# Kernel tuning notes

Hardware: AMD Instinct MI355X
Metric: run time of the kernel (lower is better)

## Reference

```python
import jax, jax.numpy as jnp
import numpy as np

HIDDEN = 1024
HEADS = 16
HEAD = HIDDEN // HEADS
B, S = 2, 2048


def setup_inputs() -> dict:
    key = jax.random.key(0)
    ks = jax.random.split(key, 8)
    query = jax.random.normal(ks[0], (B, S, HIDDEN), dtype=jnp.float32)
    key_t = jax.random.normal(ks[1], (B, S, HIDDEN), dtype=jnp.float32)
    value = jax.random.normal(ks[2], (B, S, HIDDEN), dtype=jnp.float32)
    # causal mask, broadcastable over batch and heads; 0 -> masked (-inf)
    mask = jnp.tril(jnp.ones((S, S), dtype=jnp.int32))[None, None, :, :]
    # torch Linear weights are [out_features, in_features]
    scale = 0.02
    Wq = jax.random.normal(ks[3], (HIDDEN, HIDDEN), dtype=jnp.float32) * scale
    Wk = jax.random.normal(ks[4], (HIDDEN, HIDDEN), dtype=jnp.float32) * scale
    Wv = jax.random.normal(ks[5], (HIDDEN, HIDDEN), dtype=jnp.float32) * scale
    Wo = jax.random.normal(ks[6], (HIDDEN, HIDDEN), dtype=jnp.float32) * scale
    bo = jax.random.normal(ks[7], (HIDDEN,), dtype=jnp.float32) * scale
    return {"query": query, "key": key_t, "value": value, "mask": mask,
            "Wq": Wq, "Wk": Wk, "Wv": Wv, "Wo": Wo, "bo": bo}


def reference(query, key, value, mask, Wq, Wk, Wv, Wo, bo):
    b = query.shape[0]
    # Linear (no bias): x @ W^T, then split into heads -> [b, h, s, d]
    def heads(x, W):
        y = jnp.einsum('bse,oe->bso', x, W)
        return y.reshape(b, -1, HEADS, HEAD).transpose(0, 2, 1, 3)
    Q = heads(query, Wq)
    K = heads(key, Wk)
    V = heads(value, Wv)
    inv_scale = 1.0 / jnp.sqrt(jnp.float32(HEAD))
    scores = jnp.einsum('bhqd,bhkd->bhqk', Q, K) * inv_scale  # [b,h,s,s]
    scores = jnp.where(mask == 0, -jnp.inf, scores)
    attn = jax.nn.softmax(scores, axis=-1)
    x = jnp.einsum('bhqk,bhkd->bhqd', attn, V)
    x = x.transpose(0, 2, 1, 3).reshape(b, -1, HIDDEN)
    return jnp.einsum('bse,oe->bso', x, Wo) + bo
```

## Files before the change

### kernel.cpp

```cpp
#include <hip/hip_runtime.h>


typedef __attribute__((ext_vector_type(8))) short short8;
typedef __attribute__((ext_vector_type(4))) short short4_;
typedef __attribute__((ext_vector_type(4))) float f32x4;
typedef unsigned int u32;
typedef unsigned short u16;

__device__ inline f32x4 mfma16(short8 a, short8 b, f32x4 c) {
    return __builtin_amdgcn_mfma_f32_16x16x32_bf16(a, b, c, 0, 0, 0);
}
__device__ inline u16 f2bf(float f) {
    union { float f; u32 u; } v; v.f = f;
    u32 r = v.u + 0x7fff + ((v.u >> 16) & 1);
    return (u16)(r >> 16);
}
__device__ inline void gll16(void* lds, const void* g) {
    __builtin_amdgcn_global_load_lds((const __attribute__((address_space(1))) u32*)g,
                                     (__attribute__((address_space(3))) u32*)lds,
                                     16, 0, 0);
}

__global__ __launch_bounds__(256)
void cvt_all(const float* __restrict__ q, const float* __restrict__ k,
             const float* __restrict__ v, const float* __restrict__ wq,
             const float* __restrict__ wk, const float* __restrict__ wv,
             const float* __restrict__ wo,
             u16* __restrict__ q16, u16* __restrict__ k16,
             u16* __restrict__ v16, u16* __restrict__ w16) {
    const size_t QKV = 1u << 22;
    const size_t WSZ = 1u << 20;
    size_t base = ((size_t)blockIdx.x * 256 + threadIdx.x) * 8;
    const float* src; u16* dst; size_t off; float scale = 1.0f;
    if (base < QKV)            { src = q; dst = q16; off = base;           scale = 0.125f; }
    else if (base < 2 * QKV)   { src = k; dst = k16; off = base - QKV;     }
    else if (base < 3 * QKV)   { src = v; dst = v16; off = base - 2 * QKV; }
    else {
        size_t wb = base - 3 * QKV;
        int wi = (int)(wb >> 20); off = wb & (WSZ - 1);
        src = wi == 0 ? wq : wi == 1 ? wk : wi == 2 ? wv : wo;
        dst = w16 + (size_t)wi * WSZ;
    }
    float4 f0 = *(const float4*)(src + off);
    float4 f1 = *(const float4*)(src + off + 4);
    short8 s = { (short)f2bf(f0.x * scale), (short)f2bf(f0.y * scale),
                 (short)f2bf(f0.z * scale), (short)f2bf(f0.w * scale),
                 (short)f2bf(f1.x * scale), (short)f2bf(f1.y * scale),
                 (short)f2bf(f1.z * scale), (short)f2bf(f1.w * scale) };
    *(short8*)(dst + off) = s;
}

__global__ __launch_bounds__(256)
void gemm_qkv(const u16* __restrict__ q16, const u16* __restrict__ k16,
              const u16* __restrict__ v16, const u16* __restrict__ w16,
              u16* __restrict__ Qg, u16* __restrict__ Kg, u16* __restrict__ Vt) {
    const int K = 1024;
    __shared__ u16 As[2][128 * 64];
    __shared__ u16 Bs[2][128 * 64];
    const int z = blockIdx.z;
    const u16* A = z == 0 ? q16 : z == 1 ? k16 : v16;
    const u16* W = w16 + (size_t)z * (1u << 20);

    const int tid = threadIdx.x, lane = tid & 63, w = tid >> 6;
    const int ln15 = lane & 15, quad = lane >> 4, s7 = ln15 & 7;
    const int lr = lane >> 3;
    const int lcs = (((lane & 7) ^ lr) << 3);
    const int m0 = blockIdx.y * 128, n0 = blockIdx.x * 128;
    const int wm = (w >> 1) * 64, wn = (w & 1) * 64;

    f32x4 acc[4][4] = {};

    #pragma unroll
    for (int c = 0; c < 4; ++c) {
        gll16(&As[0][(w * 32 + c * 8) * 64],
              &A[(size_t)(m0 + w * 32 + c * 8 + lr) * K + lcs]);
        gll16(&Bs[0][(w * 32 + c * 8) * 64],
              &W[(size_t)(n0 + w * 32 + c * 8 + lr) * K + lcs]);
    }

    for (int i = 0; i < 16; ++i) {
        const int cur = i & 1;
        if (i < 15) {
            const int nb = cur ^ 1, k0 = (i + 1) * 64;
            #pragma unroll
            for (int c = 0; c < 4; ++c) {
                gll16(&As[nb][(w * 32 + c * 8) * 64],
                      &A[(size_t)(m0 + w * 32 + c * 8 + lr) * K + k0 + lcs]);
                gll16(&Bs[nb][(w * 32 + c * 8) * 64],
                      &W[(size_t)(n0 + w * 32 + c * 8 + lr) * K + k0 + lcs]);
            }
            __asm__ volatile("s_waitcnt vmcnt(8)" ::: "memory");
        } else {
            __asm__ volatile("s_waitcnt vmcnt(0)" ::: "memory");
        }
        __builtin_amdgcn_s_barrier();

        #pragma unroll
        for (int kh = 0; kh < 2; ++kh) {
            short8 a[4], b[4];
            #pragma unroll
            for (int mt = 0; mt < 4; ++mt)
                a[mt] = *(const short8*)&As[cur][(wm + mt * 16 + ln15) * 64 +
                                                (((kh * 4 + quad) ^ s7) << 3)];
            #pragma unroll
            for (int nt = 0; nt < 4; ++nt)
                b[nt] = *(const short8*)&Bs[cur][(wn + nt * 16 + ln15) * 64 +
                                                (((kh * 4 + quad) ^ s7) << 3)];
            #pragma unroll
            for (int mt = 0; mt < 4; ++mt)
                #pragma unroll
                for (int nt = 0; nt < 4; ++nt)
                    acc[mt][nt] = mfma16(a[mt], b[nt], acc[mt][nt]);
        }
        __builtin_amdgcn_s_barrier();
    }

    #pragma unroll
    for (int mt = 0; mt < 4; ++mt)
        #pragma unroll
        for (int nt = 0; nt < 4; ++nt)
            #pragma unroll
            for (int r = 0; r < 4; ++r) {
                int m = m0 + wm + mt * 16 + quad * 4 + r;
                int n = n0 + wn + nt * 16 + ln15;
                u16 hv = f2bf(acc[mt][nt][r]);
                if (z == 2) {
                    int b_ = m >> 11, s_ = m & 2047, h_ = n >> 6, d_ = n & 63;
                    int kl = s_ & 63;
                    int sp = (s_ & ~63) + (kl & 15) * 4 + (kl >> 4);
                    Vt[((size_t)(b_ * 16 + h_) * 64 + d_) * 2048 + sp] = hv;
                } else {
                    u16* dst = z ? Kg : Qg;
                    dst[(size_t)m * 1024 + n] = hv;
                }
            }
}

__global__ __launch_bounds__(256)
void gemm_out(const u16* __restrict__ A, const u16* __restrict__ W,
              const float* __restrict__ bias, float* __restrict__ out) {
    const int K = 1024;
    __shared__ u16 As[2][64 * 64];
    __shared__ u16 Bs[2][128 * 64];
    const int id = blockIdx.x;
    const int by = id >> 3, bx = id & 7;

    const int tid = threadIdx.x, lane = tid & 63, w = tid >> 6;
    const int ln15 = lane & 15, quad = lane >> 4, s7 = ln15 & 7;
    const int lr = lane >> 3;
    const int lcs = (((lane & 7) ^ lr) << 3);
    const int m0 = by * 64, n0 = bx * 128;
    const int wm = (w & 1) * 32, wn = (w >> 1) * 64;

    f32x4 acc[2][4] = {};

    #pragma unroll
    for (int c = 0; c < 2; ++c)
        gll16(&As[0][(w * 16 + c * 8) * 64],
              &A[(size_t)(m0 + w * 16 + c * 8 + lr) * K + lcs]);
    #pragma unroll
    for (int c = 0; c < 4; ++c)
        gll16(&Bs[0][(w * 32 + c * 8) * 64],
              &W[(size_t)(n0 + w * 32 + c * 8 + lr) * K + lcs]);

    for (int i = 0; i < 16; ++i) {
        const int cur = i & 1;
        if (i < 15) {
            const int nb = cur ^ 1, k0 = (i + 1) * 64;
            #pragma unroll
            for (int c = 0; c < 2; ++c)
                gll16(&As[nb][(w * 16 + c * 8) * 64],
                      &A[(size_t)(m0 + w * 16 + c * 8 + lr) * K + k0 + lcs]);
            #pragma unroll
            for (int c = 0; c < 4; ++c)
                gll16(&Bs[nb][(w * 32 + c * 8) * 64],
                      &W[(size_t)(n0 + w * 32 + c * 8 + lr) * K + k0 + lcs]);
            __asm__ volatile("s_waitcnt vmcnt(6)" ::: "memory");
        } else {
            __asm__ volatile("s_waitcnt vmcnt(0)" ::: "memory");
        }
        __builtin_amdgcn_s_barrier();

        #pragma unroll
        for (int kh = 0; kh < 2; ++kh) {
            short8 a[2], b[4];
            #pragma unroll
            for (int mt = 0; mt < 2; ++mt)
                a[mt] = *(const short8*)&As[cur][(wm + mt * 16 + ln15) * 64 +
                                                (((kh * 4 + quad) ^ s7) << 3)];
            #pragma unroll
            for (int nt = 0; nt < 4; ++nt)
                b[nt] = *(const short8*)&Bs[cur][(wn + nt * 16 + ln15) * 64 +
                                                (((kh * 4 + quad) ^ s7) << 3)];
            #pragma unroll
            for (int mt = 0; mt < 2; ++mt)
                #pragma unroll
                for (int nt = 0; nt < 4; ++nt)
                    acc[mt][nt] = mfma16(a[mt], b[nt], acc[mt][nt]);
        }
        __builtin_amdgcn_s_barrier();
    }

    #pragma unroll
    for (int mt = 0; mt < 2; ++mt)
        #pragma unroll
        for (int nt = 0; nt < 4; ++nt)
            #pragma unroll
            for (int r = 0; r < 4; ++r) {
                int m = m0 + wm + mt * 16 + quad * 4 + r;
                int n = n0 + wn + nt * 16 + ln15;
                out[(size_t)m * 1024 + n] = acc[mt][nt][r] + bias[n];
            }
}

__global__ __launch_bounds__(256)
void attn3(const u16* __restrict__ Qg, const u16* __restrict__ Kg,
           const u16* __restrict__ Vt, u16* __restrict__ Xb) {
    __shared__ u16 Kl[2][64 * 64];
    __shared__ u16 Vl[2][64 * 64];
    __shared__ u16 Pl[4][16 * 72];

    const int id = blockIdx.x;
    const int bh = id & 31, qt = 31 - (id >> 5);
    const int b = bh >> 4, h = bh & 15;
    const int tid = threadIdx.x, lane = tid & 63, w = tid >> 6;
    const int ln15 = lane & 15, quad = lane >> 4, s7 = ln15 & 7;
    const int lr = lane >> 3;
    const int lcs = (((lane & 7) ^ lr) << 3);
    const u16* Kbase = Kg + (size_t)b * 2048 * 1024 + h * 64;
    const u16* Vbase = Vt + (size_t)bh * 64 * 2048;
    const float M0 = 6.0f;
    const int q0 = qt * 64;

    const u16* qrow = Qg + (size_t)(b * 2048 + q0 + w * 16 + ln15) * 1024 + h * 64;
    short8 aq0 = *(const short8*)(qrow + quad * 8);
    short8 aq1 = *(const short8*)(qrow + 32 + quad * 8);
    __asm__ volatile("s_waitcnt vmcnt(0)" ::: "memory");

    f32x4 o[4] = {};
    float lsum[4] = {0.f, 0.f, 0.f, 0.f};

    #pragma unroll
    for (int c = 0; c < 2; ++c) {
        const int r0 = w * 16 + c * 8;
        gll16(&Kl[0][r0 * 64], Kbase + (size_t)(r0 + lr) * 1024 + lcs);
        gll16(&Vl[0][r0 * 64], Vbase + (size_t)(r0 + lr) * 2048 + lcs);
    }

    for (int kt = 0; kt <= qt; ++kt) {
        const int cur = kt & 1;
        if (kt < qt) {
            const int nb = cur ^ 1, nk = (kt + 1) * 64;
            #pragma unroll
            for (int c = 0; c < 2; ++c) {
                const int r0 = w * 16 + c * 8;
                gll16(&Kl[nb][r0 * 64], Kbase + (size_t)(nk + r0 + lr) * 1024 + lcs);
                gll16(&Vl[nb][r0 * 64], Vbase + (size_t)(r0 + lr) * 2048 + nk + lcs);
            }
            __asm__ volatile("s_waitcnt vmcnt(4)" ::: "memory");
        } else {
            __asm__ volatile("s_waitcnt vmcnt(0)" ::: "memory");
        }
        __builtin_amdgcn_s_barrier();

        f32x4 sc[4];
        #pragma unroll
        for (int ct = 0; ct < 4; ++ct) {
            short8 b0 = *(const short8*)&Kl[cur][(ct * 16 + ln15) * 64 +
                                                ((quad ^ s7) << 3)];
            short8 b1 = *(const short8*)&Kl[cur][(ct * 16 + ln15) * 64 +
                                                (((4 + quad) ^ s7) << 3)];
            f32x4 c = {};
            c = mfma16(aq0, b0, c);
            c = mfma16(aq1, b1, c);
            sc[ct] = c;
        }

        const bool diag = (kt == qt);
        #pragma unroll
        for (int r = 0; r < 4; ++r) {
            float s0 = sc[0][r], s1 = sc[1][r], s2 = sc[2][r], s3 = sc[3][r];
            if (diag) {
                const int qq = w * 16 + quad * 4 + r;
                s0 = (ln15      <= qq) ? s0 : -1e30f;
                s1 = (16 + ln15 <= qq) ? s1 : -1e30f;
                s2 = (32 + ln15 <= qq) ? s2 : -1e30f;
                s3 = (48 + ln15 <= qq) ? s3 : -1e30f;
            }
            float p0 = __expf(s0 - M0), p1 = __expf(s1 - M0);
            float p2 = __expf(s2 - M0), p3 = __expf(s3 - M0);
            short4_ pw = { (short)f2bf(p0), (short)f2bf(p1),
                           (short)f2bf(p2), (short)f2bf(p3) };
            *(short4_*)&Pl[w][(quad * 4 + r) * 72 + ln15 * 4] = pw;
            lsum[r] += (p0 + p1) + (p2 + p3);
        }

        __asm__ volatile("s_waitcnt lgkmcnt(0)" ::: "memory");
        short8 ap0 = *(const short8*)&Pl[w][ln15 * 72 + quad * 8];
        short8 ap1 = *(const short8*)&Pl[w][ln15 * 72 + 32 + quad * 8];

        #pragma unroll
        for (int dt = 0; dt < 4; ++dt) {
            short8 bv0 = *(const short8*)&Vl[cur][(dt * 16 + ln15) * 64 +
                                                 ((quad ^ s7) << 3)];
            short8 bv1 = *(const short8*)&Vl[cur][(dt * 16 + ln15) * 64 +
                                                 (((4 + quad) ^ s7) << 3)];
            o[dt] = mfma16(ap0, bv0, o[dt]);
            o[dt] = mfma16(ap1, bv1, o[dt]);
        }
        __builtin_amdgcn_s_barrier();
    }

    #pragma unroll
    for (int r = 0; r < 4; ++r) {
        float l = lsum[r];
        #pragma unroll
        for (int off = 1; off < 16; off <<= 1)
            l += __shfl_xor(l, off);
        lsum[r] = l;
    }
    #pragma unroll
    for (int dt = 0; dt < 4; ++dt)
        #pragma unroll
        for (int r = 0; r < 4; ++r) {
            int q = q0 + w * 16 + quad * 4 + r;
            Xb[(size_t)(b * 2048 + q) * 1024 + h * 64 + dt * 16 + ln15] =
                f2bf(o[dt][r] / lsum[r]);
        }
}

extern "C" void kernel_launch(void* const* d_in, const int* in_sizes, int n_in,
                              void* d_out, int out_size, void* d_ws, size_t ws_size,
                              hipStream_t stream) {
    const float* query = (const float*)d_in[0];
    const float* key   = (const float*)d_in[1];
    const float* value = (const float*)d_in[2];
    const float* Wq = (const float*)d_in[4];
    const float* Wk = (const float*)d_in[5];
    const float* Wv = (const float*)d_in[6];
    const float* Wo = (const float*)d_in[7];
    const float* bo = (const float*)d_in[8];
    float* out = (float*)d_out;

    u16* ws  = (u16*)d_ws;
    const size_t T = 1ull << 22;
    u16* q16 = ws;
    u16* k16 = ws + T;
    u16* v16 = ws + 2 * T;
    u16* w16 = ws + 3 * T;
    u16* Qg  = ws + 4 * T;
    u16* Kg  = ws + 5 * T;
    u16* Vt  = (u16*)d_out;
    u16* Xb  = q16;
    const size_t WSZ = 1ull << 20;

    cvt_all<<<8192, 256, 0, stream>>>(query, key, value, Wq, Wk, Wv, Wo,
                                      q16, k16, v16, w16);

    gemm_qkv<<<dim3(8, 32, 3), 256, 0, stream>>>(q16, k16, v16, w16, Qg, Kg, Vt);

    attn3<<<1024, 256, 0, stream>>>(Qg, Kg, Vt, Xb);

    gemm_out<<<512, 256, 0, stream>>>(Xb, w16 + 3 * WSZ, bo, out);
}
```

Baseline: 230.9 us.

## Process two query tiles per attention block to reuse K/V tiles

Each attention workgroup now handles 128 query rows (two 64-row subtiles) instead of 64, so every K/V tile loaded into LDS is used by both subtiles. This halves the grid to 512 blocks and roughly halves global K/V traffic and load/barrier overhead per query row. The trade-off is fewer blocks for load balancing on a causal workload, more registers for the doubled accumulators, and serialized subtile work within each tile iteration.

```diff
diff --git a/kernel.cpp b/kernel.cpp
--- a/kernel.cpp
+++ b/kernel.cpp
@@ -214,14 +214,14 @@
 }
 
 __global__ __launch_bounds__(256)
-void attn3(const u16* __restrict__ Qg, const u16* __restrict__ Kg,
+void attn5(const u16* __restrict__ Qg, const u16* __restrict__ Kg,
            const u16* __restrict__ Vt, u16* __restrict__ Xb) {
     __shared__ u16 Kl[2][64 * 64];
     __shared__ u16 Vl[2][64 * 64];
     __shared__ u16 Pl[4][16 * 72];
 
     const int id = blockIdx.x;
-    const int bh = id & 31, qt = 31 - (id >> 5);
+    const int bh = id & 31, qt = 15 - (id >> 5);
     const int b = bh >> 4, h = bh & 15;
     const int tid = threadIdx.x, lane = tid & 63, w = tid >> 6;
     const int ln15 = lane & 15, quad = lane >> 4, s7 = ln15 & 7;
@@ -230,15 +230,20 @@
     const u16* Kbase = Kg + (size_t)b * 2048 * 1024 + h * 64;
     const u16* Vbase = Vt + (size_t)bh * 64 * 2048;
     const float M0 = 6.0f;
-    const int q0 = qt * 64;
-
-    const u16* qrow = Qg + (size_t)(b * 2048 + q0 + w * 16 + ln15) * 1024 + h * 64;
-    short8 aq0 = *(const short8*)(qrow + quad * 8);
-    short8 aq1 = *(const short8*)(qrow + 32 + quad * 8);
+    const int q0 = qt * 128;
+    const int lastkt = 2 * qt + 1;
+
+    short8 aq[2][2];
+    #pragma unroll
+    for (int s = 0; s < 2; ++s) {
+        const u16* qrow = Qg + (size_t)(b * 2048 + q0 + s * 64 + w * 16 + ln15) * 1024 + h * 64;
+        aq[s][0] = *(const short8*)(qrow + quad * 8);
+        aq[s][1] = *(const short8*)(qrow + 32 + quad * 8);
+    }
     __asm__ volatile("s_waitcnt vmcnt(0)" ::: "memory");
 
-    f32x4 o[4] = {};
-    float lsum[4] = {0.f, 0.f, 0.f, 0.f};
+    f32x4 o[2][4] = {};
+    float lsum[2][4] = {};
 
     #pragma unroll
     for (int c = 0; c < 2; ++c) {
@@ -247,9 +252,9 @@
         gll16(&Vl[0][r0 * 64], Vbase + (size_t)(r0 + lr) * 2048 + lcs);
     }
 
-    for (int kt = 0; kt <= qt; ++kt) {
+    for (int kt = 0; kt <= lastkt; ++kt) {
         const int cur = kt & 1;
-        if (kt < qt) {
+        if (kt < lastkt) {
             const int nb = cur ^ 1, nk = (kt + 1) * 64;
             #pragma unroll
             for (int c = 0; c < 2; ++c) {
@@ -263,70 +268,78 @@
         }
         __builtin_amdgcn_s_barrier();
 
-        f32x4 sc[4];
-        #pragma unroll
-        for (int ct = 0; ct < 4; ++ct) {
-            short8 b0 = *(const short8*)&Kl[cur][(ct * 16 + ln15) * 64 +
-                                                ((quad ^ s7) << 3)];
-            short8 b1 = *(const short8*)&Kl[cur][(ct * 16 + ln15) * 64 +
-                                                (((4 + quad) ^ s7) << 3)];
-            f32x4 c = {};
-            c = mfma16(aq0, b0, c);
-            c = mfma16(aq1, b1, c);
-            sc[ct] = c;
-        }
-
-        const bool diag = (kt == qt);
+        #pragma unroll
+        for (int s = 0; s < 2; ++s) {
+            if (s == 0 && kt == lastkt) continue;
+
+            f32x4 sc[4];
+            #pragma unroll
+            for (int ct = 0; ct < 4; ++ct) {
+                short8 b0 = *(const short8*)&Kl[cur][(ct * 16 + ln15) * 64 +
+                                                    ((quad ^ s7) << 3)];
+                short8 b1 = *(const short8*)&Kl[cur][(ct * 16 + ln15) * 64 +
+                                                    (((4 + quad) ^ s7) << 3)];
+                f32x4 c = {};
+                c = mfma16(aq[s][0], b0, c);
+                c = mfma16(aq[s][1], b1, c);
+                sc[ct] = c;
+            }
+
+            const bool diag = (kt == 2 * qt + s);
+            #pragma unroll
+            for (int r = 0; r < 4; ++r) {
+                float s0 = sc[0][r], s1 = sc[1][r], s2 = sc[2][r], s3 = sc[3][r];
+                if (diag) {
+                    const int qq = w * 16 + quad * 4 + r;
+                    s0 = (ln15      <= qq) ? s0 : -1e30f;
+                    s1 = (16 + ln15 <= qq) ? s1 : -1e30f;
+                    s2 = (32 + ln15 <= qq) ? s2 : -1e30f;
+                    s3 = (48 + ln15 <= qq) ? s3 : -1e30f;
+                }
+                float p0 = __expf(s0 - M0), p1 = __expf(s1 - M0);
+                float p2 = __expf(s2 - M0), p3 = __expf(s3 - M0);
+                short4_ pw = { (short)f2bf(p0), (short)f2bf(p1),
+                               (short)f2bf(p2), (short)f2bf(p3) };
+                *(short4_*)&Pl[w][(quad * 4 + r) * 72 + ln15 * 4] = pw;
+                lsum[s][r] += (p0 + p1) + (p2 + p3);
+            }
+
+            __asm__ volatile("s_waitcnt lgkmcnt(0)" ::: "memory");
+            short8 ap0 = *(const short8*)&Pl[w][ln15 * 72 + quad * 8];
+            short8 ap1 = *(const short8*)&Pl[w][ln15 * 72 + 32 + quad * 8];
+
+            #pragma unroll
+            for (int dt = 0; dt < 4; ++dt) {
+                short8 bv0 = *(const short8*)&Vl[cur][(dt * 16 + ln15) * 64 +
+                                                     ((quad ^ s7) << 3)];
+                short8 bv1 = *(const short8*)&Vl[cur][(dt * 16 + ln15) * 64 +
+                                                     (((4 + quad) ^ s7) << 3)];
+                o[s][dt] = mfma16(ap0, bv0, o[s][dt]);
+                o[s][dt] = mfma16(ap1, bv1, o[s][dt]);
+            }
+        }
+        __builtin_amdgcn_s_barrier();
+    }
+
+    #pragma unroll
+    for (int s = 0; s < 2; ++s) {
         #pragma unroll
         for (int r = 0; r < 4; ++r) {
-            float s0 = sc[0][r], s1 = sc[1][r], s2 = sc[2][r], s3 = sc[3][r];
-            if (diag) {
-                const int qq = w * 16 + quad * 4 + r;
-                s0 = (ln15      <= qq) ? s0 : -1e30f;
-                s1 = (16 + ln15 <= qq) ? s1 : -1e30f;
-                s2 = (32 + ln15 <= qq) ? s2 : -1e30f;
-                s3 = (48 + ln15 <= qq) ? s3 : -1e30f;
-            }
-            float p0 = __expf(s0 - M0), p1 = __expf(s1 - M0);
-            float p2 = __expf(s2 - M0), p3 = __expf(s3 - M0);
-            short4_ pw = { (short)f2bf(p0), (short)f2bf(p1),
-                           (short)f2bf(p2), (short)f2bf(p3) };
-            *(short4_*)&Pl[w][(quad * 4 + r) * 72 + ln15 * 4] = pw;
-            lsum[r] += (p0 + p1) + (p2 + p3);
-        }
-
-        __asm__ volatile("s_waitcnt lgkmcnt(0)" ::: "memory");
-        short8 ap0 = *(const short8*)&Pl[w][ln15 * 72 + quad * 8];
-        short8 ap1 = *(const short8*)&Pl[w][ln15 * 72 + 32 + quad * 8];
-
-        #pragma unroll
-        for (int dt = 0; dt < 4; ++dt) {
-            short8 bv0 = *(const short8*)&Vl[cur][(dt * 16 + ln15) * 64 +
-                                                 ((quad ^ s7) << 3)];
-            short8 bv1 = *(const short8*)&Vl[cur][(dt * 16 + ln15) * 64 +
-                                                 (((4 + quad) ^ s7) << 3)];
-            o[dt] = mfma16(ap0, bv0, o[dt]);
-            o[dt] = mfma16(ap1, bv1, o[dt]);
-        }
-        __builtin_amdgcn_s_barrier();
-    }
-
-    #pragma unroll
-    for (int r = 0; r < 4; ++r) {
-        float l = lsum[r];
-        #pragma unroll
-        for (int off = 1; off < 16; off <<= 1)
-            l += __shfl_xor(l, off);
-        lsum[r] = l;
-    }
-    #pragma unroll
-    for (int dt = 0; dt < 4; ++dt)
-        #pragma unroll
-        for (int r = 0; r < 4; ++r) {
-            int q = q0 + w * 16 + quad * 4 + r;
-            Xb[(size_t)(b * 2048 + q) * 1024 + h * 64 + dt * 16 + ln15] =
-                f2bf(o[dt][r] / lsum[r]);
-        }
+            float l = lsum[s][r];
+            #pragma unroll
+            for (int off = 1; off < 16; off <<= 1)
+                l += __shfl_xor(l, off);
+            lsum[s][r] = l;
+        }
+        #pragma unroll
+        for (int dt = 0; dt < 4; ++dt)
+            #pragma unroll
+            for (int r = 0; r < 4; ++r) {
+                int q = q0 + s * 64 + w * 16 + quad * 4 + r;
+                Xb[(size_t)(b * 2048 + q) * 1024 + h * 64 + dt * 16 + ln15] =
+                    f2bf(o[s][dt][r] / lsum[s][r]);
+            }
+    }
 }
 
 extern "C" void kernel_launch(void* const* d_in, const int* in_sizes, int n_in,
@@ -359,7 +372,7 @@
 
     gemm_qkv<<<dim3(8, 32, 3), 256, 0, stream>>>(q16, k16, v16, w16, Qg, Kg, Vt);
 
-    attn3<<<1024, 256, 0, stream>>>(Qg, Kg, Vt, Xb);
+    attn5<<<512, 256, 0, stream>>>(Qg, Kg, Vt, Xb);
 
     gemm_out<<<512, 256, 0, stream>>>(Xb, w16 + 3 * WSZ, bo, out);
 }
```

Measured after the change: 257.0 us. 11.3% more time.
